# Performance work log

Measured on AMD Instinct MI355X. Metric: run time of the kernel, lower is better.

The kernel has to match this reference:

```python
import jax, jax.numpy as jnp
import numpy as np

B, L, C, N, TN = 1, 256, 128, 4, 4
CH = N * C  # 512, flattened hidden for routing projections
EPS = 1.1920929e-07  # torch.finfo(float32).eps (RMSNorm default eps)
LN_EPS = 1e-5
N_SINKHORN = 20  # training-mode iteration count


def sinkhorn_knopp(raw, n_iters):
    # raw: [..., n, n] real-valued logits -> doubly-stochastic matrix
    M = jnp.exp(raw)
    for _ in range(n_iters):
        M = M / jnp.sum(M, axis=-1, keepdims=True)  # row normalize
        M = M / jnp.sum(M, axis=-2, keepdims=True)  # col normalize
    return M


def setup_inputs() -> dict:
    key = jax.random.key(0)
    ks = jax.random.split(key, 8)
    s = 0.02
    eye = jnp.eye(N, dtype=jnp.float32)
    b_res = 2.0 * eye + (-2.0) * (1.0 - eye)
    return {
        "p": jax.random.normal(ks[0], (B, L, L, C), jnp.float32),
        "p_mask": jnp.ones((B, L, L), jnp.float32),
        "W_pre": jax.random.normal(ks[1], (N, CH), jnp.float32) * s,
        "W_post": jax.random.normal(ks[2], (N, CH), jnp.float32) * s,
        "W_res": jax.random.normal(ks[3], (N * N, CH), jnp.float32) * s,
        "b_pre": jnp.zeros((1, N), jnp.float32),
        "b_post": jnp.zeros((1, N), jnp.float32),
        "b_res": b_res,
        "alpha_pre": jnp.asarray(0.01, jnp.float32),
        "alpha_post": jnp.asarray(0.01, jnp.float32),
        "alpha_res": jnp.asarray(0.01, jnp.float32),
        "ln_g": jnp.ones((C,), jnp.float32),
        "ln_b": jnp.zeros((C,), jnp.float32),
        "W1": jax.random.normal(ks[4], (TN * C, C), jnp.float32) * s,
        "b1": jnp.zeros((TN * C,), jnp.float32),
        "W2": jax.random.normal(ks[5], (C, TN * C), jnp.float32) * s,
        "b2": jnp.zeros((C,), jnp.float32),
    }


def reference(p, p_mask, W_pre, W_post, W_res, b_pre, b_post, b_res,
              alpha_pre, alpha_post, alpha_res, ln_g, ln_b, W1, b1, W2, b2):
    # expand_input: [B,L,L,C] -> [B,L,L,n,C]
    x = jnp.broadcast_to(p[..., None, :], (B, L, L, N, C))
    # --- compute_mappings ---
    xf = x.reshape(B, L, L, CH)
    xn = xf * jax.lax.rsqrt(jnp.mean(xf * xf, axis=-1, keepdims=True) + EPS)
    H_pre_dyn = jnp.tanh(xn @ W_pre.T)                      # [B,L,L,n]
    H_post_dyn = jnp.tanh(xn @ W_post.T)                    # [B,L,L,n]
    H_res_dyn = jnp.tanh(xn @ W_res.T).reshape(B, L, L, N, N)
    H_pre = jax.nn.sigmoid(alpha_pre * H_pre_dyn + b_pre)   # [B,L,L,n]
    H_post = 2.0 * jax.nn.sigmoid(alpha_post * H_post_dyn + b_post)
    H_res = sinkhorn_knopp(alpha_res * H_res_dyn + b_res, N_SINKHORN)  # [B,L,L,n,n]
    # contract: H_pre [B,L,L,1,n] @ x [B,L,L,n,C] -> [B,L,L,C]
    p_c = jnp.einsum('blkn,blknc->blkc', H_pre, x)
    # --- PairTransition (LN -> Linear -> ReLU -> Linear, masked) ---
    mu = jnp.mean(p_c, axis=-1, keepdims=True)
    var = jnp.mean(jnp.square(p_c - mu), axis=-1, keepdims=True)
    m = (p_c - mu) * jax.lax.rsqrt(var + LN_EPS) * ln_g + ln_b
    h = jax.nn.relu(m @ W1.T + b1)                          # [B,L,L,TN*C]
    p_t = (h @ W2.T + b2) * p_mask[..., None]
    p_updated = p_c + p_t
    # expand back: H_post^T [B,L,L,n,1] * p_updated [B,L,L,1,C]
    p_expanded = H_post[..., :, None] * p_updated[..., None, :]
    # residual mixing: [B,L,L,n,n] @ [B,L,L,n,C]
    p_residual = jnp.einsum('blkmn,blknc->blkmc', H_res, x)
    return p_residual + p_expanded  # [B,L,L,n,C]
```

## Files before the change

### kernel.cpp

```cpp
#include <hip/hip_runtime.h>
#include <stdint.h>

#define LLTOT 65536
#define CDIM  128
#define TPIX  32

typedef float f32x4  __attribute__((ext_vector_type(4)));
typedef float f32x16 __attribute__((ext_vector_type(16)));
typedef short s16x8  __attribute__((ext_vector_type(8)));

#define MFMA16(a, b, c) __builtin_amdgcn_mfma_f32_16x16x32_bf16((a), (b), (c), 0, 0, 0)
#define MFMA32(a, b, c) __builtin_amdgcn_mfma_f32_32x32x16_bf16((a), (b), (c), 0, 0, 0)

#define RPAD 132

__device__ __align__(16) unsigned short g_wefff[2 * 4 * 64 * 8];
__device__ __align__(16) unsigned short g_w1gf[32 * 4 * 64 * 8];
__device__ __align__(16) unsigned short g_w2f [4 * 32 * 64 * 8];
__device__ __align__(16) float  g_hA[512];
__device__ __align__(16) float  g_w1gs[512];

__device__ __forceinline__ unsigned short f2bf(float f) {
    union { float f; uint32_t u; } v; v.f = f;
    uint32_t u = v.u;
    return (unsigned short)((u + 0x7FFFu + ((u >> 16) & 1u)) >> 16);
}
__device__ __forceinline__ uint32_t pack2(float a, float b) {
    uint32_t r;
    asm("v_cvt_pk_bf16_f32 %0, %1, %2" : "=v"(r) : "v"(a), "v"(b));
    return r;
}
__device__ __forceinline__ float bf2f(uint32_t lo16) { return __uint_as_float(lo16 << 16); }

__device__ __forceinline__ float fast_tanh(float x) {
    float cx = fminf(fmaxf(x, -10.f), 10.f);
    float e = __expf(2.f * cx);
    return (e - 1.f) * __builtin_amdgcn_rcpf(e + 1.f);
}
__device__ __forceinline__ float fast_sig(float z) {
    return __builtin_amdgcn_rcpf(1.f + __expf(-z));
}

__global__ void prep_kernel(const float* __restrict__ Wpre, const float* __restrict__ Wpost,
                            const float* __restrict__ Wres, const float* __restrict__ W1,
                            const float* __restrict__ W2, const float* __restrict__ ln_g,
                            const float* __restrict__ ln_b, const float* __restrict__ b1) {
    int b = blockIdx.x, t = threadIdx.x;
    if (b == 264) {
        int j = t;
        float sg = 0.f, sb = 0.f;
        const float* row = W1 + j * 128;
        #pragma unroll 4
        for (int c = 0; c < 128; c += 4) {
            float4 wv = *(const float4*)(row + c);
            float4 gv = *(const float4*)(ln_g + c);
            float4 bv = *(const float4*)(ln_b + c);
            sg += wv.x*gv.x + wv.y*gv.y + wv.z*gv.z + wv.w*gv.w;
            sb += wv.x*bv.x + wv.y*bv.y + wv.z*bv.z + wv.w*bv.w;
        }
        g_hA[j]   = b1[j] + sb;
        g_w1gs[j] = sg;
        return;
    }
    int idx = b * 512 + t;
    if (idx < 4096) {
        int e = idx & 7, lane = (idx >> 3) & 63, kk = (idx >> 9) & 3, tile = idx >> 11;
        int o = tile * 16 + (lane & 15);
        int c = kk * 32 + (lane >> 4) * 8 + e;
        float v = 0.f;
        if (o < 4)        v = Wpre[o*512+c] + Wpre[o*512+128+c] + Wpre[o*512+256+c] + Wpre[o*512+384+c];
        else if (o < 8)   { int j = o - 4;  v = Wpost[j*512+c] + Wpost[j*512+128+c] + Wpost[j*512+256+c] + Wpost[j*512+384+c]; }
        else if (o < 24)  { int j = o - 8;  v = Wres[j*512+c] + Wres[j*512+128+c] + Wres[j*512+256+c] + Wres[j*512+384+c]; }
        g_wefff[idx] = f2bf(v);
    } else if (idx < 69632) {
        int d = idx - 4096;
        int e = d & 7, lane = (d >> 3) & 63, kk = (d >> 9) & 3, jt = d >> 11;
        int j = jt * 16 + (lane & 15);
        int c = kk * 32 + (lane >> 4) * 8 + e;
        g_w1gf[d] = f2bf(W1[j * 128 + c] * ln_g[c]);
    } else if (idx < 135168) {
        int d = idx - 69632;
        int e = d & 7, lane = (d >> 3) & 63, kk = (d >> 9) & 31, ct = (d >> 14) & 3;
        int c = ct * 32 + (lane & 31);
        int k = kk * 16 + (lane >> 5) * 8 + e;
        g_w2f[d] = f2bf(W2[c * 512 + k]);
    }
}

__global__ void __launch_bounds__(512, 2) fused_kernel(
    const float* __restrict__ p, const float* __restrict__ p_mask,
    const float* __restrict__ b_pre, const float* __restrict__ b_post, const float* __restrict__ b_res,
    const float* __restrict__ a_pre, const float* __restrict__ a_post, const float* __restrict__ a_res,
    const float* __restrict__ b2g, float* __restrict__ out)
{
    __shared__ __align__(16) unsigned short pf_lds[8 * 64 * 8];
    __shared__ __align__(16) unsigned short h32[32 * 64 * 8];
    __shared__ __align__(16) float redA[32 * RPAD];
    __shared__ __align__(16) float redB[32 * RPAD];
    __shared__ __align__(16) float A_s[128], B_s[128];
    __shared__ __align__(16) float2 simi_s[32];

    const int t = threadIdx.x;
    const int w = t >> 6, l = t & 63, lr = l & 15, lk = l >> 4;
    const size_t base = (size_t)blockIdx.x * TPIX;

    float M0 = 0.f, M1 = 0.f, M2 = 0.f, M3 = 0.f, sp = 0.f, hpm = 0.f;
    int mrow = 0, pix = 0;

    if (w < 2) {
        const int g = lk, pixl = lr;
        const size_t gpix = base + w * 16 + pixl;
        float apre = a_pre[0], apost = a_post[0], ares = a_res[0];
        float msk = p_mask[gpix];
        float bp0 = b_pre[0], bp1 = b_pre[1], bp2 = b_pre[2], bp3 = b_pre[3];
        float bq0 = b_post[0], bq1 = b_post[1], bq2 = b_post[2], bq3 = b_post[3];
        mrow = (g + 2) & 3;
        float br0 = b_res[mrow*4+0], br1 = b_res[mrow*4+1], br2 = b_res[mrow*4+2], br3 = b_res[mrow*4+3];

        float s = 0.f, ss = 0.f;
        s16x8 pf[4];
        const float* prow = p + gpix * 128 + g * 8;
        #pragma unroll
        for (int kk = 0; kk < 4; ++kk) {
            float4 va = *(const float4*)(prow + kk * 32);
            float4 vb = *(const float4*)(prow + kk * 32 + 4);
            s  += va.x + va.y + va.z + va.w + vb.x + vb.y + vb.z + vb.w;
            ss += va.x*va.x + va.y*va.y + va.z*va.z + va.w*va.w
                + vb.x*vb.x + vb.y*vb.y + vb.z*vb.z + vb.w*vb.w;
            union { s16x8 v; uint32_t u[4]; } cc;
            cc.u[0] = pack2(va.x, va.y);
            cc.u[1] = pack2(va.z, va.w);
            cc.u[2] = pack2(vb.x, vb.y);
            cc.u[3] = pack2(vb.z, vb.w);
            pf[kk] = cc.v;
            *(s16x8*)(pf_lds + (size_t)(w * 4 + kk) * 512 + l * 8) = cc.v;
        }
        s  += __shfl_xor(s, 16);  ss += __shfl_xor(ss, 16);
        s  += __shfl_xor(s, 32);  ss += __shfl_xor(ss, 32);
        float mu = s * (1.f / 128.f), mq = ss * (1.f / 128.f);
        float rv  = rsqrtf(mq + 1.1920929e-07f);
        float var = mq - mu * mu;

        f32x4 y1 = {0.f, 0.f, 0.f, 0.f}, y2 = {0.f, 0.f, 0.f, 0.f};
        #pragma unroll
        for (int kk = 0; kk < 4; ++kk) {
            s16x8 a0 = *(const s16x8*)(g_wefff + ((size_t)(kk) * 64 + l) * 8);
            s16x8 a1 = *(const s16x8*)(g_wefff + ((size_t)(4 + kk) * 64 + l) * 8);
            y1 = MFMA16(a0, pf[kk], y1);
            y2 = MFMA16(a1, pf[kk], y2);
        }
        #pragma unroll
        for (int r = 0; r < 4; ++r) { y1[r] *= rv; y2[r] *= rv; }

        float sp_loc = fast_sig(apre * fast_tanh(y1[0]) + bp0)
                     + fast_sig(apre * fast_tanh(y1[1]) + bp1)
                     + fast_sig(apre * fast_tanh(y1[2]) + bp2)
                     + fast_sig(apre * fast_tanh(y1[3]) + bp3);
        sp = __shfl(sp_loc, pixl);

        float hp0 = 2.f * fast_sig(apost * fast_tanh(y1[0]) + bq0);
        float hp1 = 2.f * fast_sig(apost * fast_tanh(y1[1]) + bq1);
        float hp2 = 2.f * fast_sig(apost * fast_tanh(y1[2]) + bq2);
        float hp3 = 2.f * fast_sig(apost * fast_tanh(y1[3]) + bq3);

        bool lo = g < 2;
        M0 = __expf(ares * fast_tanh(lo ? y2[0] : y1[0]) + br0);
        M1 = __expf(ares * fast_tanh(lo ? y2[1] : y1[1]) + br1);
        M2 = __expf(ares * fast_tanh(lo ? y2[2] : y1[2]) + br2);
        M3 = __expf(ares * fast_tanh(lo ? y2[3] : y1[3]) + br3);

        float h0b = __shfl(hp0, pixl + 16);
        float h1b = __shfl(hp1, pixl + 16);
        float h2b = __shfl(hp2, pixl + 16);
        float h3b = __shfl(hp3, pixl + 16);
        hpm = (mrow & 2) ? ((mrow & 1) ? h3b : h2b) : ((mrow & 1) ? h1b : h0b);

        pix = w * 16 + pixl;
        B_s[pix * 4 + mrow] = hpm * msk;
        if (l < 16) {
            float istd = rsqrtf(sp * sp * var + 1e-5f);
            simi_s[pix] = make_float2(sp * istd, sp * mu * istd);
        }
    }
    __syncthreads();

    if (w < 2) {
        #pragma unroll 1
        for (int it = 0; it < 20; ++it) {
            float ri = __builtin_amdgcn_rcpf(M0 + M1 + M2 + M3);
            M0 *= ri; M1 *= ri; M2 *= ri; M3 *= ri;
            float c0 = M0, c1 = M1, c2 = M2, c3 = M3;
            c0 += __shfl_xor(c0, 16); c1 += __shfl_xor(c1, 16); c2 += __shfl_xor(c2, 16); c3 += __shfl_xor(c3, 16);
            c0 += __shfl_xor(c0, 32); c1 += __shfl_xor(c1, 32); c2 += __shfl_xor(c2, 32); c3 += __shfl_xor(c3, 32);
            M0 *= __builtin_amdgcn_rcpf(c0); M1 *= __builtin_amdgcn_rcpf(c1);
            M2 *= __builtin_amdgcn_rcpf(c2); M3 *= __builtin_amdgcn_rcpf(c3);
        }
        float rm = M0 + M1 + M2 + M3;
        A_s[pix * 4 + mrow] = rm + hpm * sp;
    }

    s16x8 pfr[2][4];
    #pragma unroll
    for (int it = 0; it < 2; ++it)
        #pragma unroll
        for (int kk = 0; kk < 4; ++kk)
            pfr[it][kk] = *(const s16x8*)(pf_lds + (size_t)(it * 4 + kk) * 512 + l * 8);

    f32x4 acc1[4][2] = {};
    #pragma unroll
    for (int kk = 0; kk < 4; ++kk)
        #pragma unroll
        for (int jt = 0; jt < 4; ++jt) {
            s16x8 a = *(const s16x8*)(g_w1gf + ((size_t)((w * 4 + jt) * 4 + kk) * 64 + l) * 8);
            acc1[jt][0] = MFMA16(a, pfr[0][kk], acc1[jt][0]);
            acc1[jt][1] = MFMA16(a, pfr[1][kk], acc1[jt][1]);
        }

    {
        float2 sim0 = simi_s[lr];
        float2 sim1 = simi_s[16 + lr];
        #pragma unroll
        for (int jt = 0; jt < 4; ++jt) {
            int j0 = w * 64 + jt * 16 + lk * 4;
            float4 wg = *(const float4*)(g_w1gs + j0);
            float4 ha = *(const float4*)(g_hA + j0);
            #pragma unroll
            for (int it = 0; it < 2; ++it) {
                float si = it ? sim1.x : sim0.x;
                float mi = it ? sim1.y : sim0.y;
                f32x4 v = acc1[jt][it];
                float h0 = fmaxf(fmaf(si, v[0], fmaf(-mi, wg.x, ha.x)), 0.f);
                float h1 = fmaxf(fmaf(si, v[1], fmaf(-mi, wg.y, ha.y)), 0.f);
                float h2 = fmaxf(fmaf(si, v[2], fmaf(-mi, wg.z, ha.z)), 0.f);
                float h3 = fmaxf(fmaf(si, v[3], fmaf(-mi, wg.w, ha.w)), 0.f);
                uint2 uu;
                uu.x = pack2(h0, h1);
                uu.y = pack2(h2, h3);
                uint32_t addr = (uint32_t)((w * 4 + jt) * 1024
                              + (it * 16 + lr + 32 * (lk >> 1)) * 16 + (lk & 1) * 8);
                *(uint2*)((char*)h32 + addr) = uu;
            }
        }
    }
    __syncthreads();

    {
        const int ct = w & 3, kh = w >> 2;
        f32x16 acc2 = {0.f,0.f,0.f,0.f, 0.f,0.f,0.f,0.f, 0.f,0.f,0.f,0.f, 0.f,0.f,0.f,0.f};
        #pragma unroll 4
        for (int kk2 = 0; kk2 < 16; ++kk2) {
            int ks = kh * 16 + kk2;
            s16x8 a = *(const s16x8*)(g_w2f + ((size_t)(ct * 32 + ks) * 64 + l) * 8);
            s16x8 b = *(const s16x8*)(h32 + (size_t)ks * 512 + l * 8);
            acc2 = MFMA32(a, b, acc2);
        }
        float* red = kh ? redB : redA;
        int pixd = l & 31;
        #pragma unroll
        for (int q = 0; q < 4; ++q) {
            f32x4 v = {acc2[4*q+0], acc2[4*q+1], acc2[4*q+2], acc2[4*q+3]};
            int c = ct * 32 + 8 * q + 4 * (l >> 5);
            *(f32x4*)(red + pixd * RPAD + c) = v;
        }
    }
    __syncthreads();

    const int c0 = w * 16 + lk * 4;
    float4 b2v = *(const float4*)(b2g + c0);
    #pragma unroll
    for (int it = 0; it < 2; ++it) {
        int i = it * 16 + lr;
        f32x4 Av = *(const f32x4*)(A_s + i * 4);
        f32x4 Bv = *(const f32x4*)(B_s + i * 4);
        f32x4 Da = *(const f32x4*)(redA + i * RPAD + c0);
        f32x4 Db = *(const f32x4*)(redB + i * RPAD + c0);
        const unsigned short* pe = pf_lds
            + ((size_t)(it * 4 + (w >> 1)) * 64 + ((w & 1) * 2 + (lk >> 1)) * 16 + lr) * 8
            + (lk & 1) * 4;
        uint2 pb = *(const uint2*)pe;
        float p0 = bf2f(pb.x & 0xffffu), p1 = __uint_as_float(pb.x & 0xffff0000u);
        float p2 = bf2f(pb.y & 0xffffu), p3 = __uint_as_float(pb.y & 0xffff0000u);
        float d0 = Da[0] + Db[0] + b2v.x;
        float d1 = Da[1] + Db[1] + b2v.y;
        float d2 = Da[2] + Db[2] + b2v.z;
        float d3 = Da[3] + Db[3] + b2v.w;
        float* og = out + (base + i) * 512 + c0;
        #pragma unroll
        for (int m = 0; m < 4; ++m) {
            f32x4 o;
            o[0] = Av[m] * p0 + Bv[m] * d0;
            o[1] = Av[m] * p1 + Bv[m] * d1;
            o[2] = Av[m] * p2 + Bv[m] * d2;
            o[3] = Av[m] * p3 + Bv[m] * d3;
            *(f32x4*)(og + m * 128) = o;
        }
    }
}

extern "C" void kernel_launch(void* const* d_in, const int* in_sizes, int n_in,
                              void* d_out, int out_size, void* d_ws, size_t ws_size,
                              hipStream_t stream) {
    const float* p      = (const float*)d_in[0];
    const float* p_mask = (const float*)d_in[1];
    const float* W_pre  = (const float*)d_in[2];
    const float* W_post = (const float*)d_in[3];
    const float* W_res  = (const float*)d_in[4];
    const float* b_pre  = (const float*)d_in[5];
    const float* b_post = (const float*)d_in[6];
    const float* b_res  = (const float*)d_in[7];
    const float* a_pre  = (const float*)d_in[8];
    const float* a_post = (const float*)d_in[9];
    const float* a_res  = (const float*)d_in[10];
    const float* ln_g   = (const float*)d_in[11];
    const float* ln_b   = (const float*)d_in[12];
    const float* W1     = (const float*)d_in[13];
    const float* b1     = (const float*)d_in[14];
    const float* W2     = (const float*)d_in[15];
    const float* b2     = (const float*)d_in[16];
    float* out = (float*)d_out;

    prep_kernel<<<265, 512, 0, stream>>>(W_pre, W_post, W_res, W1, W2, ln_g, ln_b, b1);
    fused_kernel<<<2048, 512, 0, stream>>>(p, p_mask, b_pre, b_post, b_res,
                                           a_pre, a_post, a_res, b2, out);
}
```

Baseline: 74.14 us.

## Spread input load and RMS stats across all waves, prefetch first W1 fragments

Before, only the first two waves loaded the 32-pixel tile of p, computed the mean and RMS statistics, and packed it to bf16 in LDS. Now all 512 threads load p cooperatively, reduce the stats with 16-lane shuffles, write them to shared arrays, and fill the LDS fragment layout before a new barrier. The routing waves then read their B fragments and stats from LDS. Every wave also preloads the first half of its W1 weight fragments into registers at kernel start so those global loads overlap the prologue. The cost is an extra __syncthreads and more register pressure under the 512-thread, 2-block launch bound.

```diff
diff --git a/kernel.cpp b/kernel.cpp
--- a/kernel.cpp
+++ b/kernel.cpp
@@ -99,10 +99,47 @@
     __shared__ __align__(16) float redB[32 * RPAD];
     __shared__ __align__(16) float A_s[128], B_s[128];
     __shared__ __align__(16) float2 simi_s[32];
+    __shared__ __align__(16) float rms_s[32], mu_s[32], var_s[32];
 
     const int t = threadIdx.x;
     const int w = t >> 6, l = t & 63, lr = l & 15, lk = l >> 4;
     const size_t base = (size_t)blockIdx.x * TPIX;
+
+    s16x8 aw01[8];
+    #pragma unroll
+    for (int kk = 0; kk < 2; ++kk)
+        #pragma unroll
+        for (int jt = 0; jt < 4; ++jt)
+            aw01[kk * 4 + jt] = *(const s16x8*)(g_w1gf + ((size_t)((w * 4 + jt) * 4 + kk) * 64 + l) * 8);
+
+    {
+        int pix32 = t >> 4, ci = t & 15;
+        const float* src = p + (base + pix32) * 128 + ci * 8;
+        float4 va = *(const float4*)src;
+        float4 vb = *(const float4*)(src + 4);
+        float s  = va.x + va.y + va.z + va.w + vb.x + vb.y + vb.z + vb.w;
+        float ss = va.x*va.x + va.y*va.y + va.z*va.z + va.w*va.w
+                 + vb.x*vb.x + vb.y*vb.y + vb.z*vb.z + vb.w*vb.w;
+        s += __shfl_xor(s, 1); ss += __shfl_xor(ss, 1);
+        s += __shfl_xor(s, 2); ss += __shfl_xor(ss, 2);
+        s += __shfl_xor(s, 4); ss += __shfl_xor(ss, 4);
+        s += __shfl_xor(s, 8); ss += __shfl_xor(ss, 8);
+        if (ci == 0) {
+            float mu = s * (1.f / 128.f), mq = ss * (1.f / 128.f);
+            rms_s[pix32] = rsqrtf(mq + 1.1920929e-07f);
+            mu_s[pix32]  = mu;
+            var_s[pix32] = mq - mu * mu;
+        }
+        uint4 u;
+        u.x = pack2(va.x, va.y);
+        u.y = pack2(va.z, va.w);
+        u.z = pack2(vb.x, vb.y);
+        u.w = pack2(vb.z, vb.w);
+        uint32_t a16 = (uint32_t)((((pix32 >> 4) * 4 + (ci >> 2)) * 512
+                     + ((pix32 & 15) + 16 * (ci & 3)) * 8));
+        *(uint4*)(pf_lds + a16) = u;
+    }
+    __syncthreads();
 
     float M0 = 0.f, M1 = 0.f, M2 = 0.f, M3 = 0.f, sp = 0.f, hpm = 0.f;
     int mrow = 0, pix = 0;
@@ -117,37 +154,16 @@
         mrow = (g + 2) & 3;
         float br0 = b_res[mrow*4+0], br1 = b_res[mrow*4+1], br2 = b_res[mrow*4+2], br3 = b_res[mrow*4+3];
 
-        float s = 0.f, ss = 0.f;
-        s16x8 pf[4];
-        const float* prow = p + gpix * 128 + g * 8;
+        float rv = rms_s[w * 16 + pixl];
+
+        f32x4 y1 = {0.f, 0.f, 0.f, 0.f}, y2 = {0.f, 0.f, 0.f, 0.f};
         #pragma unroll
         for (int kk = 0; kk < 4; ++kk) {
-            float4 va = *(const float4*)(prow + kk * 32);
-            float4 vb = *(const float4*)(prow + kk * 32 + 4);
-            s  += va.x + va.y + va.z + va.w + vb.x + vb.y + vb.z + vb.w;
-            ss += va.x*va.x + va.y*va.y + va.z*va.z + va.w*va.w
-                + vb.x*vb.x + vb.y*vb.y + vb.z*vb.z + vb.w*vb.w;
-            union { s16x8 v; uint32_t u[4]; } cc;
-            cc.u[0] = pack2(va.x, va.y);
-            cc.u[1] = pack2(va.z, va.w);
-            cc.u[2] = pack2(vb.x, vb.y);
-            cc.u[3] = pack2(vb.z, vb.w);
-            pf[kk] = cc.v;
-            *(s16x8*)(pf_lds + (size_t)(w * 4 + kk) * 512 + l * 8) = cc.v;
-        }
-        s  += __shfl_xor(s, 16);  ss += __shfl_xor(ss, 16);
-        s  += __shfl_xor(s, 32);  ss += __shfl_xor(ss, 32);
-        float mu = s * (1.f / 128.f), mq = ss * (1.f / 128.f);
-        float rv  = rsqrtf(mq + 1.1920929e-07f);
-        float var = mq - mu * mu;
-
-        f32x4 y1 = {0.f, 0.f, 0.f, 0.f}, y2 = {0.f, 0.f, 0.f, 0.f};
-        #pragma unroll
-        for (int kk = 0; kk < 4; ++kk) {
+            s16x8 bfr = *(const s16x8*)(pf_lds + (size_t)(w * 4 + kk) * 512 + l * 8);
             s16x8 a0 = *(const s16x8*)(g_wefff + ((size_t)(kk) * 64 + l) * 8);
             s16x8 a1 = *(const s16x8*)(g_wefff + ((size_t)(4 + kk) * 64 + l) * 8);
-            y1 = MFMA16(a0, pf[kk], y1);
-            y2 = MFMA16(a1, pf[kk], y2);
+            y1 = MFMA16(a0, bfr, y1);
+            y2 = MFMA16(a1, bfr, y2);
         }
         #pragma unroll
         for (int r = 0; r < 4; ++r) { y1[r] *= rv; y2[r] *= rv; }
@@ -178,8 +194,9 @@
         pix = w * 16 + pixl;
         B_s[pix * 4 + mrow] = hpm * msk;
         if (l < 16) {
-            float istd = rsqrtf(sp * sp * var + 1e-5f);
-            simi_s[pix] = make_float2(sp * istd, sp * mu * istd);
+            int px = w * 16 + lr;
+            float istd = rsqrtf(sp * sp * var_s[px] + 1e-5f);
+            simi_s[px] = make_float2(sp * istd, sp * mu_s[px] * istd);
         }
     }
     __syncthreads();
@@ -208,7 +225,15 @@
 
     f32x4 acc1[4][2] = {};
     #pragma unroll
-    for (int kk = 0; kk < 4; ++kk)
+    for (int kk = 0; kk < 2; ++kk)
+        #pragma unroll
+        for (int jt = 0; jt < 4; ++jt) {
+            s16x8 a = aw01[kk * 4 + jt];
+            acc1[jt][0] = MFMA16(a, pfr[0][kk], acc1[jt][0]);
+            acc1[jt][1] = MFMA16(a, pfr[1][kk], acc1[jt][1]);
+        }
+    #pragma unroll
+    for (int kk = 2; kk < 4; ++kk)
         #pragma unroll
         for (int jt = 0; jt < 4; ++jt) {
             s16x8 a = *(const s16x8*)(g_w1gf + ((size_t)((w * 4 + jt) * 4 + kk) * 64 + l) * 8);
```

New measurement: 71.07 us. -4.1%, faster.
